# Performance work log

Measured on AMD Instinct MI355X. Metric: run time of the kernel, lower is better.

## Reference

```python
import jax, jax.numpy as jnp
import numpy as np

N = 30000      # nodes
E = 300000     # directed edges (self loops added in conv)
G = 128        # graphs in the batch
IN = 128       # input_dim
HID = 64       # hidden per head
HEADS = 4
NC = 10        # num_classes
EPS = 1e-5
SLOPE = 0.2    # GATv2 leaky_relu negative slope


def setup_inputs() -> dict:
    key = jax.random.key(0)
    ks = jax.random.split(key, 40)
    d = {}
    d['x'] = jax.random.normal(ks[0], (N, IN), jnp.float32)
    d['edge_index'] = jax.random.randint(ks[1], (2, E), 0, N, jnp.int32)
    d['batch'] = jnp.sort(jax.random.randint(ks[2], (N,), 0, G, jnp.int32))
    in_ch = [IN, HID * HEADS, HID * HEADS, HID * HEADS]
    for i in range(4):
        oc = HID * HEADS if i < 3 else HID  # last layer concat=False -> HID
        sc = 1.0 / np.sqrt(in_ch[i])
        d[f'Wl{i}'] = jax.random.normal(ks[3 + 6 * i], (in_ch[i], HID * HEADS), jnp.float32) * sc
        d[f'Wr{i}'] = jax.random.normal(ks[4 + 6 * i], (in_ch[i], HID * HEADS), jnp.float32) * sc
        d[f'att{i}'] = jax.random.normal(ks[5 + 6 * i], (HEADS, HID), jnp.float32) * 0.1
        d[f'b{i}'] = jnp.zeros((oc,), jnp.float32)
        d[f'bng{i}'] = jnp.ones((oc,), jnp.float32)
        d[f'bnb{i}'] = jnp.zeros((oc,), jnp.float32)
    d['fc1_w'] = jax.random.normal(ks[30], (HID, HID), jnp.float32) / np.sqrt(HID)
    d['fc1_b'] = jnp.zeros((HID,), jnp.float32)
    d['fc2_w'] = jax.random.normal(ks[31], (HID, NC), jnp.float32) / np.sqrt(HID)
    d['fc2_b'] = jnp.zeros((NC,), jnp.float32)
    return d


def _gatv2_conv(h, src, dst, Wl, Wr, att, b, concat):
    # GATv2Conv: x_l = lin_l(x) for sources, x_r = lin_r(x) for targets
    xl = (h @ Wl).reshape(N, HEADS, HID)
    xr = (h @ Wr).reshape(N, HEADS, HID)
    z = jax.nn.leaky_relu(xl[src] + xr[dst], SLOPE)       # [Et, H, C]
    e = jnp.einsum('ehc,hc->eh', z, att)                   # [Et, H]
    m = jax.ops.segment_max(e, dst, num_segments=N)        # per-dst max
    p = jnp.exp(e - m[dst])
    s = jax.ops.segment_sum(p, dst, num_segments=N)
    alpha = p / s[dst]                                     # segment softmax
    msg = alpha[..., None] * xl[src]                       # [Et, H, C]
    out = jax.ops.segment_sum(msg, dst, num_segments=N)    # [N, H, C]
    out = out.reshape(N, HEADS * HID) if concat else out.mean(axis=1)
    return out + b


def _bn_train(h, g, b):
    mu = h.mean(axis=0)
    var = h.var(axis=0)  # biased, as torch BN uses for normalization
    return g * (h - mu) * jax.lax.rsqrt(var + EPS) + b


def _forward(x, edge_index, batch,
             Wl0, Wr0, att0, b0, bng0, bnb0,
             Wl1, Wr1, att1, b1, bng1, bnb1,
             Wl2, Wr2, att2, b2, bng2, bnb2,
             Wl3, Wr3, att3, b3, bng3, bnb3,
             fc1_w, fc1_b, fc2_w, fc2_b):
    loops = jnp.arange(N, dtype=edge_index.dtype)
    src = jnp.concatenate([edge_index[0], loops])  # add_self_loops=True
    dst = jnp.concatenate([edge_index[1], loops])
    layers = [(Wl0, Wr0, att0, b0, bng0, bnb0, True),
              (Wl1, Wr1, att1, b1, bng1, bnb1, True),
              (Wl2, Wr2, att2, b2, bng2, bnb2, True),
              (Wl3, Wr3, att3, b3, bng3, bnb3, False)]
    h = x
    for Wl, Wr, att, b, g, bb, concat in layers:
        h = jax.nn.elu(_bn_train(_gatv2_conv(h, src, dst, Wl, Wr, att, b, concat), g, bb))
    sums = jax.ops.segment_sum(h, batch, num_segments=G)
    cnt = jax.ops.segment_sum(jnp.ones((N,), h.dtype), batch, num_segments=G)
    pooled = sums / jnp.maximum(cnt, 1.0)[:, None]         # global_mean_pool
    o = jax.nn.relu(pooled @ fc1_w + fc1_b)
    return o @ fc2_w + fc2_b                               # dropout off (eval)


def reference(x, edge_index, batch,
              Wl0, Wr0, att0, b0, bng0, bnb0,
              Wl1, Wr1, att1, b1, bng1, bnb1,
              Wl2, Wr2, att2, b2, bng2, bnb2,
              Wl3, Wr3, att3, b3, bng3, bnb3,
              fc1_w, fc1_b, fc2_w, fc2_b):
    return _forward(x, edge_index, batch,
                    Wl0, Wr0, att0, b0, bng0, bnb0,
                    Wl1, Wr1, att1, b1, bng1, bnb1,
                    Wl2, Wr2, att2, b2, bng2, bnb2,
                    Wl3, Wr3, att3, b3, bng3, bnb3,
                    fc1_w, fc1_b, fc2_w, fc2_b)
```

## Files before the change

kernel.cpp:

```cpp
#include <hip/hip_runtime.h>
#include <hip/hip_bf16.h>
#include <math.h>

#define NN    30000
#define EE    300000
#define ETOT  330000
#define GG    128
#define IND   128
#define HIDD  64
#define NHEAD 4
#define CC    256
#define NCL   10
#define EPSBN 1e-5f
#define SLOPE 0.2f

typedef __attribute__((ext_vector_type(8))) __bf16 bf16x8;
typedef __attribute__((ext_vector_type(4))) float f32x4;

__device__ inline float b2f(unsigned u16) {
    union { unsigned i; float f; } c; c.i = u16 << 16; return c.f;
}
__device__ inline unsigned short f2b(float f) {
    __hip_bfloat16 b = __float2bfloat16(f);
    unsigned short u; __builtin_memcpy(&u, &b, 2); return u;
}
__device__ inline void unpack8(uint4 u, float* f) {
    f[0] = b2f(u.x & 0xffffu); f[1] = b2f(u.x >> 16);
    f[2] = b2f(u.y & 0xffffu); f[3] = b2f(u.y >> 16);
    f[4] = b2f(u.z & 0xffffu); f[5] = b2f(u.z >> 16);
    f[6] = b2f(u.w & 0xffffu); f[7] = b2f(u.w >> 16);
}

__global__ void k_deg(const int* __restrict__ ei, int* __restrict__ deg) {
    int e = blockIdx.x * blockDim.x + threadIdx.x;
    if (e >= ETOT) return;
    int d = (e < EE) ? ei[EE + e] : (e - EE);
    atomicAdd(&deg[d], 1);
}

__global__ void k_scan(const int* __restrict__ deg, int* __restrict__ rowptr,
                       int* __restrict__ cursor) {
    const int PER = 30;
    int t = threadIdx.x;
    int base = t * PER;
    int loc[PER];
    int s = 0;
    #pragma unroll
    for (int j = 0; j < PER; ++j) {
        int v = (base + j < NN) ? deg[base + j] : 0;
        loc[j] = s; s += v;
    }
    int lane = t & 63, wid = t >> 6;
    int v = s;
    #pragma unroll
    for (int d = 1; d < 64; d <<= 1) {
        int u = __shfl_up(v, d, 64);
        if (lane >= d) v += u;
    }
    __shared__ int wsum[16], woff[16];
    if (lane == 63) wsum[wid] = v;
    __syncthreads();
    if (t == 0) { int a = 0; for (int w2 = 0; w2 < 16; ++w2) { woff[w2] = a; a += wsum[w2]; } }
    __syncthreads();
    int excl = woff[wid] + (v - s);
    #pragma unroll
    for (int j = 0; j < PER; ++j) {
        int idx = base + j;
        if (idx <= NN) { int val = excl + loc[j]; rowptr[idx] = val; cursor[idx] = val; }
    }
}

__global__ void k_scatter(const int* __restrict__ ei, int* __restrict__ cursor,
                          int* __restrict__ csrc) {
    int e = blockIdx.x * blockDim.x + threadIdx.x;
    if (e >= ETOT) return;
    int s, d;
    if (e < EE) { s = ei[e]; d = ei[EE + e]; } else { s = e - EE; d = s; }
    int pos = atomicAdd(&cursor[d], 1);
    csrc[pos] = s;
}

struct WPtrs { const float* wl[4]; const float* wr[4]; };

__global__ void k_prep(WPtrs p, const float* __restrict__ x,
                       __hip_bfloat16* __restrict__ wt, __hip_bfloat16* __restrict__ hb) {
    int id = blockIdx.x * 256 + threadIdx.x;
    if (id < 65536) {
        int n = id >> 7, k = id & 127;
        float v = (n < 256) ? p.wl[0][(size_t)k * 256 + n] : p.wr[0][(size_t)k * 256 + n - 256];
        wt[id] = __float2bfloat16(v);
    } else if (id < 458752) {
        int id2 = id - 65536;
        int li = 1 + (id2 >> 17);
        int r = id2 & 131071;
        int n = r >> 8, k = r & 255;
        float v = (n < 256) ? p.wl[li][(size_t)k * 256 + n] : p.wr[li][(size_t)k * 256 + n - 256];
        wt[id] = __float2bfloat16(v);
    } else {
        int id2 = id - 458752;
        if (id2 < NN * IND) hb[id2] = __float2bfloat16(x[id2]);
    }
}

template<int K>
__global__ __launch_bounds__(256) void k_gemm_mfma(
        const __hip_bfloat16* __restrict__ A, const __hip_bfloat16* __restrict__ Wt,
        __hip_bfloat16* __restrict__ xlb, __hip_bfloat16* __restrict__ xrb) {
    __shared__ __bf16 As[128 * 40];
    __shared__ __bf16 Bs[128 * 40];
    const int t = threadIdx.x;
    const int row0 = blockIdx.x * 128;
    const int col0 = blockIdx.y * 128;
    const int wv = t >> 6, lane = t & 63;
    const int wm = (wv & 1) * 64, wn = (wv >> 1) * 64;
    const int lm = lane & 15, lq = lane >> 4;
    f32x4 acc[4][4] = {};
    for (int k0 = 0; k0 < K; k0 += 32) {
        #pragma unroll
        for (int i = 0; i < 2; ++i) {
            int c = i * 256 + t;
            int r = c >> 2, cc = (c & 3) * 8;
            uint4 v = make_uint4(0u, 0u, 0u, 0u);
            int gr = row0 + r;
            if (gr < NN) v = *(const uint4*)&A[(size_t)gr * K + k0 + cc];
            *(uint4*)&As[r * 40 + cc] = v;
            uint4 w = *(const uint4*)&Wt[(size_t)(col0 + r) * K + k0 + cc];
            *(uint4*)&Bs[r * 40 + cc] = w;
        }
        __syncthreads();
        bf16x8 af[4], bfr[4];
        #pragma unroll
        for (int i = 0; i < 4; ++i) {
            af[i]  = *(bf16x8*)&As[(wm + i * 16 + lm) * 40 + lq * 8];
            bfr[i] = *(bf16x8*)&Bs[(wn + i * 16 + lm) * 40 + lq * 8];
        }
        #pragma unroll
        for (int i = 0; i < 4; ++i)
            #pragma unroll
            for (int j = 0; j < 4; ++j)
                acc[i][j] = __builtin_amdgcn_mfma_f32_16x16x32_bf16(af[i], bfr[j], acc[i][j], 0, 0, 0);
        __syncthreads();
    }
    const int crow = (lane >> 4) * 4;
    const int ccol = lane & 15;
    #pragma unroll
    for (int j = 0; j < 4; ++j) {
        int gcol = col0 + wn + j * 16 + ccol;
        __hip_bfloat16* O = (gcol < 256) ? xlb : xrb;
        int oc = (gcol < 256) ? gcol : gcol - 256;
        #pragma unroll
        for (int i = 0; i < 4; ++i) {
            #pragma unroll
            for (int r = 0; r < 4; ++r) {
                int grow = row0 + wm + i * 16 + crow + r;
                if (grow < NN) O[(size_t)grow * CC + oc] = __float2bfloat16(acc[i][j][r]);
            }
        }
    }
}

template<bool CONCAT>
__global__ __launch_bounds__(256) void k_gat(const __hip_bfloat16* __restrict__ xlb,
        const __hip_bfloat16* __restrict__ xrb, const int* __restrict__ rowptr,
        const int* __restrict__ csrc, const float* __restrict__ att,
        __hip_bfloat16* __restrict__ outb, float* __restrict__ outf) {
    const int wv = threadIdx.x >> 6, lane = threadIdx.x & 63;
    const int n = blockIdx.x * 4 + wv;
    if (n >= NN) return;
    const int sub = lane >> 5, l5 = lane & 31;
    const float4* att4 = (const float4*)att;
    float4 a0 = att4[l5 * 2], a1 = att4[l5 * 2 + 1];
    float aw[8] = {a0.x, a0.y, a0.z, a0.w, a1.x, a1.y, a1.z, a1.w};
    const uint4* xl4 = (const uint4*)xlb;
    const uint4* xr4 = (const uint4*)xrb;
    float xrv[8]; unpack8(xr4[(size_t)n * 32 + l5], xrv);
    const int beg = rowptr[n], end = rowptr[n + 1];
    float m = -1e30f, ssum = 0.f;
    float acc[8] = {};
    for (int i0 = beg; i0 < end; i0 += 2) {
        int i = i0 + sub;
        bool valid = i < end;
        int s = csrc[valid ? i : (end - 1)];
        float xlv[8]; unpack8(xl4[(size_t)s * 32 + l5], xlv);
        float tv = 0.f;
        #pragma unroll
        for (int j = 0; j < 8; ++j) {
            float v = xlv[j] + xrv[j];
            v = fmaxf(v, SLOPE * v);
            tv += v * aw[j];
        }
        tv += __shfl_xor(tv, 1);
        tv += __shfl_xor(tv, 2);
        tv += __shfl_xor(tv, 4);
        if (!valid) tv = -1e38f;
        float mn = fmaxf(m, tv);
        float sc = __expf(m - mn);
        float p  = __expf(tv - mn);
        ssum = ssum * sc + p;
        #pragma unroll
        for (int j = 0; j < 8; ++j) acc[j] = acc[j] * sc + p * xlv[j];
        m = mn;
    }
    float om = __shfl_xor(m, 32);
    float mn = fmaxf(m, om);
    float sa = __expf(m - mn), sb = __expf(om - mn);
    float osum = __shfl_xor(ssum, 32);
    ssum = ssum * sa + osum * sb;
    #pragma unroll
    for (int j = 0; j < 8; ++j) {
        float oa = __shfl_xor(acc[j], 32);
        acc[j] = acc[j] * sa + oa * sb;
    }
    float inv = 1.f / ssum;
    if (CONCAT) {
        if (sub == 0) {
            unsigned short r[8];
            #pragma unroll
            for (int j = 0; j < 8; ++j) r[j] = f2b(acc[j] * inv);
            uint4 o;
            o.x = r[0] | ((unsigned)r[1] << 16); o.y = r[2] | ((unsigned)r[3] << 16);
            o.z = r[4] | ((unsigned)r[5] << 16); o.w = r[6] | ((unsigned)r[7] << 16);
            ((uint4*)outb)[(size_t)n * 32 + l5] = o;
        }
    } else {
        float v[8];
        #pragma unroll
        for (int j = 0; j < 8; ++j) {
            v[j] = acc[j] * inv;
            v[j] += __shfl_xor(v[j], 8);
            v[j] += __shfl_xor(v[j], 16);
            v[j] *= 0.25f;
        }
        if (lane < 8) {
            ((float4*)outf)[(size_t)n * 16 + lane * 2]     = make_float4(v[0], v[1], v[2], v[3]);
            ((float4*)outf)[(size_t)n * 16 + lane * 2 + 1] = make_float4(v[4], v[5], v[6], v[7]);
        }
    }
}

__global__ __launch_bounds__(256) void k_bnstats256b(const __hip_bfloat16* __restrict__ in,
                                                     float* __restrict__ stats) {
    __shared__ float sh[512];
    int r0 = blockIdx.x * 128;
    int rend = min(r0 + 128, NN);
    int t = threadIdx.x;
    int half = t >> 7, tc = t & 127;
    float s0 = 0.f, s1 = 0.f, q0 = 0.f, q1 = 0.f;
    const unsigned* u32 = (const unsigned*)in;
    for (int r = r0 + half; r < rend; r += 2) {
        unsigned w = u32[(size_t)r * 128 + tc];
        float a = b2f(w & 0xffffu), b = b2f(w >> 16);
        s0 += a; q0 += a * a; s1 += b; q1 += b * b;
    }
    if (half) {
        sh[tc * 4 + 0] = s0; sh[tc * 4 + 1] = s1;
        sh[tc * 4 + 2] = q0; sh[tc * 4 + 3] = q1;
    }
    __syncthreads();
    if (!half) {
        s0 += sh[tc * 4 + 0]; s1 += sh[tc * 4 + 1];
        q0 += sh[tc * 4 + 2]; q1 += sh[tc * 4 + 3];
        atomicAdd(&stats[2 * tc], s0);       atomicAdd(&stats[2 * tc + 1], s1);
        atomicAdd(&stats[256 + 2 * tc], q0); atomicAdd(&stats[256 + 2 * tc + 1], q1);
    }
}

__global__ __launch_bounds__(256) void k_bnelu256b(const __hip_bfloat16* __restrict__ in,
        const float* __restrict__ stats, const float* __restrict__ gamma,
        const float* __restrict__ beta, __hip_bfloat16* __restrict__ outb) {
    int id = blockIdx.x * 256 + threadIdx.x;
    if (id >= NN * 32) return;
    int c0 = (id & 31) * 8;
    uint4 u = ((const uint4*)in)[id];
    float f[8]; unpack8(u, f);
    unsigned short r[8];
    #pragma unroll
    for (int j = 0; j < 8; ++j) {
        int c = c0 + j;
        float mu  = stats[c] * (1.f / NN);
        float var = stats[256 + c] * (1.f / NN) - mu * mu;
        float w = gamma[c] * rsqrtf(var + EPSBN);
        float v = w * (f[j] - mu) + beta[c];
        v = (v > 0.f) ? v : (__expf(v) - 1.f);
        r[j] = f2b(v);
    }
    uint4 o;
    o.x = r[0] | ((unsigned)r[1] << 16); o.y = r[2] | ((unsigned)r[3] << 16);
    o.z = r[4] | ((unsigned)r[5] << 16); o.w = r[6] | ((unsigned)r[7] << 16);
    ((uint4*)outb)[id] = o;
}

__global__ void k_bnstats64(const float* __restrict__ h, float* __restrict__ stats) {
    int r0 = blockIdx.x * 128;
    int rend = min(r0 + 128, NN);
    int c = threadIdx.x & 63;
    int ro = threadIdx.x >> 6;
    float s = 0.f, q = 0.f;
    for (int r = r0 + ro; r < rend; r += 4) {
        float v = h[(size_t)r * 64 + c];
        s += v; q += v * v;
    }
    atomicAdd(&stats[c], s); atomicAdd(&stats[64 + c], q);
}

__global__ void k_bnelu64(const float* __restrict__ in, const float* __restrict__ stats,
        const float* __restrict__ gamma, const float* __restrict__ beta,
        float* __restrict__ outf) {
    int i = blockIdx.x * blockDim.x + threadIdx.x;
    if (i >= NN * 64) return;
    int c = i & 63;
    float mu  = stats[c] * (1.f / NN);
    float var = stats[64 + c] * (1.f / NN) - mu * mu;
    float w = gamma[c] * rsqrtf(var + EPSBN);
    float v = w * (in[i] - mu) + beta[c];
    outf[i] = (v > 0.f) ? v : (__expf(v) - 1.f);
}

__global__ void k_pool(const float* __restrict__ h, const int* __restrict__ batch,
                       float* __restrict__ pooled, float* __restrict__ cnt) {
    int wv = threadIdx.x >> 6, lane = threadIdx.x & 63;
    int w = blockIdx.x * 4 + wv;
    int n0 = w * 64;
    if (n0 >= NN) return;
    int n1 = min(n0 + 64, NN);
    float sum = 0.f;
    int cur = batch[n0], c = 0;
    for (int n = n0; n < n1; ++n) {
        int g = batch[n];
        if (g != cur) {
            atomicAdd(&pooled[cur * 64 + lane], sum);
            if (lane == 0) atomicAdd(&cnt[cur], (float)c);
            sum = 0.f; c = 0; cur = g;
        }
        sum += h[(size_t)n * 64 + lane];
        ++c;
    }
    atomicAdd(&pooled[cur * 64 + lane], sum);
    if (lane == 0) atomicAdd(&cnt[cur], (float)c);
}

__global__ void k_mlp(const float* __restrict__ pooled, const float* __restrict__ cnt,
        const float* __restrict__ w1, const float* __restrict__ b1,
        const float* __restrict__ w2, const float* __restrict__ b2,
        float* __restrict__ out) {
    __shared__ float p[64], o[64];
    int g = blockIdx.x, t = threadIdx.x;
    float c = fmaxf(cnt[g], 1.f);
    p[t] = pooled[g * 64 + t] / c;
    __syncthreads();
    float s = b1[t];
    for (int k = 0; k < 64; ++k) s += p[k] * w1[k * 64 + t];
    o[t] = fmaxf(s, 0.f);
    __syncthreads();
    if (t < NCL) {
        float s2 = b2[t];
        for (int k = 0; k < 64; ++k) s2 += o[k] * w2[k * NCL + t];
        out[g * NCL + t] = s2;
    }
}

extern "C" void kernel_launch(void* const* d_in, const int* in_sizes, int n_in,
                              void* d_out, int out_size, void* d_ws, size_t ws_size,
                              hipStream_t stream) {
    const float* x     = (const float*)d_in[0];
    const int*   ei    = (const int*)d_in[1];
    const int*   batch = (const int*)d_in[2];
    WPtrs wp;
    const float *attp[4], *bng[4], *bnb[4];
    for (int i = 0; i < 4; ++i) {
        wp.wl[i] = (const float*)d_in[3 + 6 * i];
        wp.wr[i] = (const float*)d_in[4 + 6 * i];
        attp[i]  = (const float*)d_in[5 + 6 * i];
        bng[i]   = (const float*)d_in[7 + 6 * i];
        bnb[i]   = (const float*)d_in[8 + 6 * i];
    }
    const float* fc1w = (const float*)d_in[27];
    const float* fc1b = (const float*)d_in[28];
    const float* fc2w = (const float*)d_in[29];
    const float* fc2b = (const float*)d_in[30];
    float* out = (float*)d_out;

    char* w = (char*)d_ws;
    __hip_bfloat16* xlb = (__hip_bfloat16*)w; w += (size_t)NN * CC * 2;
    __hip_bfloat16* xrb = (__hip_bfloat16*)w; w += (size_t)NN * CC * 2;
    __hip_bfloat16* bufB = (__hip_bfloat16*)w; w += (size_t)NN * CC * 2;
    __hip_bfloat16* hb   = (__hip_bfloat16*)w; w += (size_t)NN * CC * 2;
    __hip_bfloat16* wt   = (__hip_bfloat16*)w; w += (size_t)458752 * 2;
    float* bufF   = (float*)w; w += (size_t)NN * HIDD * 4;
    float* bufA   = (float*)w; w += (size_t)NN * HIDD * 4;
    int*   rowptr = (int*)w;   w += (size_t)(NN + 1) * 4;
    int*   cursor = (int*)w;   w += (size_t)(NN + 1) * 4;
    int*   csrc   = (int*)w;   w += (size_t)ETOT * 4;
    char* zbase = w;
    int*   deg       = (int*)w;   w += (size_t)NN * 4;
    float* stats_all = (float*)w; w += (size_t)4 * 512 * 4;
    float* pooled    = (float*)w; w += (size_t)GG * HIDD * 4;
    float* cnt       = (float*)w; w += (size_t)GG * 4;
    size_t zbytes = (size_t)(w - zbase);

    __hip_bfloat16* Wt[4];
    Wt[0] = wt;
    Wt[1] = wt + 65536;
    Wt[2] = wt + 65536 + 131072;
    Wt[3] = wt + 65536 + 262144;

    hipMemsetAsync(zbase, 0, zbytes, stream);
    k_deg<<<(ETOT + 255) / 256, 256, 0, stream>>>(ei, deg);
    k_scan<<<1, 1024, 0, stream>>>(deg, rowptr, cursor);
    k_scatter<<<(ETOT + 255) / 256, 256, 0, stream>>>(ei, cursor, csrc);
    k_prep<<<(458752 + NN * IND + 255) / 256, 256, 0, stream>>>(wp, x, wt, hb);

    for (int L = 0; L < 4; ++L) {
        float* stats = stats_all + 512 * L;
        dim3 gg((NN + 127) / 128, 4);
        if (L == 0) k_gemm_mfma<IND><<<gg, 256, 0, stream>>>(hb, Wt[0], xlb, xrb);
        else        k_gemm_mfma<CC><<<gg, 256, 0, stream>>>(hb, Wt[L], xlb, xrb);
        if (L < 3) {
            k_gat<true><<<NN / 4, 256, 0, stream>>>(xlb, xrb, rowptr, csrc, attp[L], bufB, nullptr);
            k_bnstats256b<<<(NN + 127) / 128, 256, 0, stream>>>(bufB, stats);
            k_bnelu256b<<<(NN * 32 + 255) / 256, 256, 0, stream>>>(bufB, stats, bng[L], bnb[L], hb);
        } else {
            k_gat<false><<<NN / 4, 256, 0, stream>>>(xlb, xrb, rowptr, csrc, attp[3], nullptr, bufF);
            k_bnstats64<<<(NN + 127) / 128, 256, 0, stream>>>(bufF, stats);
            k_bnelu64<<<(NN * 64 + 255) / 256, 256, 0, stream>>>(bufF, stats, bng[3], bnb[3], bufA);
        }
    }
    k_pool<<<((NN + 63) / 64 + 3) / 4, 256, 0, stream>>>(bufA, batch, pooled, cnt);
    k_mlp<<<GG, 64, 0, stream>>>(pooled, cnt, fc1w, fc1b, fc2w, fc2b, out);
}
```

Measured before the change: 622.0 us.

## Prefetch GEMM tiles, drop softmax max-tracking, fuse final BN-ELU into pooling

The GEMM now prefetches the next K-slice into registers while the current one computes. Its buffers are padded to a multiple of 128 rows so the row bounds checks can be dropped, and the xl/xr output pointer is chosen once per block. The GAT kernel stops tracking a running max for the online softmax and sums exp(e) directly, which removes the rescaling exps and multiplies. This risks overflow if attention logits are large. The final BN+ELU is folded into the pooling kernel, which removes one elementwise kernel launch and one intermediate buffer.

```diff
diff --git a/kernel.cpp b/kernel.cpp
--- a/kernel.cpp
+++ b/kernel.cpp
@@ -3,6 +3,7 @@
 #include <math.h>
 
 #define NN    30000
+#define MPAD  30080
 #define EE    300000
 #define ETOT  330000
 #define GG    128
@@ -114,20 +115,27 @@
     const int wv = t >> 6, lane = t & 63;
     const int wm = (wv & 1) * 64, wn = (wv >> 1) * 64;
     const int lm = lane & 15, lq = lane >> 4;
+    const int sr0 = t >> 2, scc = (t & 3) * 8;
+    const int sr1 = sr0 + 64;
+    uint4 va0, va1, vb0, vb1;
+    va0 = *(const uint4*)&A [(size_t)(row0 + sr0) * K + scc];
+    va1 = *(const uint4*)&A [(size_t)(row0 + sr1) * K + scc];
+    vb0 = *(const uint4*)&Wt[(size_t)(col0 + sr0) * K + scc];
+    vb1 = *(const uint4*)&Wt[(size_t)(col0 + sr1) * K + scc];
     f32x4 acc[4][4] = {};
     for (int k0 = 0; k0 < K; k0 += 32) {
-        #pragma unroll
-        for (int i = 0; i < 2; ++i) {
-            int c = i * 256 + t;
-            int r = c >> 2, cc = (c & 3) * 8;
-            uint4 v = make_uint4(0u, 0u, 0u, 0u);
-            int gr = row0 + r;
-            if (gr < NN) v = *(const uint4*)&A[(size_t)gr * K + k0 + cc];
-            *(uint4*)&As[r * 40 + cc] = v;
-            uint4 w = *(const uint4*)&Wt[(size_t)(col0 + r) * K + k0 + cc];
-            *(uint4*)&Bs[r * 40 + cc] = w;
-        }
+        *(uint4*)&As[sr0 * 40 + scc] = va0;
+        *(uint4*)&As[sr1 * 40 + scc] = va1;
+        *(uint4*)&Bs[sr0 * 40 + scc] = vb0;
+        *(uint4*)&Bs[sr1 * 40 + scc] = vb1;
         __syncthreads();
+        if (k0 + 32 < K) {
+            int kn = k0 + 32;
+            va0 = *(const uint4*)&A [(size_t)(row0 + sr0) * K + kn + scc];
+            va1 = *(const uint4*)&A [(size_t)(row0 + sr1) * K + kn + scc];
+            vb0 = *(const uint4*)&Wt[(size_t)(col0 + sr0) * K + kn + scc];
+            vb1 = *(const uint4*)&Wt[(size_t)(col0 + sr1) * K + kn + scc];
+        }
         bf16x8 af[4], bfr[4];
         #pragma unroll
         for (int i = 0; i < 4; ++i) {
@@ -141,20 +149,18 @@
                 acc[i][j] = __builtin_amdgcn_mfma_f32_16x16x32_bf16(af[i], bfr[j], acc[i][j], 0, 0, 0);
         __syncthreads();
     }
-    const int crow = (lane >> 4) * 4;
-    const int ccol = lane & 15;
+    const int crow = lq * 4;
+    __hip_bfloat16* O = (blockIdx.y < 2) ? xlb : xrb;
+    const int cbase = (blockIdx.y & 1) * 128 + wn;
     #pragma unroll
     for (int j = 0; j < 4; ++j) {
-        int gcol = col0 + wn + j * 16 + ccol;
-        __hip_bfloat16* O = (gcol < 256) ? xlb : xrb;
-        int oc = (gcol < 256) ? gcol : gcol - 256;
+        int oc = cbase + j * 16 + lm;
         #pragma unroll
         for (int i = 0; i < 4; ++i) {
+            int grow = row0 + wm + i * 16 + crow;
             #pragma unroll
-            for (int r = 0; r < 4; ++r) {
-                int grow = row0 + wm + i * 16 + crow + r;
-                if (grow < NN) O[(size_t)grow * CC + oc] = __float2bfloat16(acc[i][j][r]);
-            }
+            for (int r = 0; r < 4; ++r)
+                O[(size_t)(grow + r) * CC + oc] = __float2bfloat16(acc[i][j][r]);
         }
     }
 }
@@ -175,42 +181,31 @@
     const uint4* xr4 = (const uint4*)xrb;
     float xrv[8]; unpack8(xr4[(size_t)n * 32 + l5], xrv);
     const int beg = rowptr[n], end = rowptr[n + 1];
-    float m = -1e30f, ssum = 0.f;
+    float ssum = 0.f;
     float acc[8] = {};
     for (int i0 = beg; i0 < end; i0 += 2) {
         int i = i0 + sub;
         bool valid = i < end;
-        int s = csrc[valid ? i : (end - 1)];
+        int s = csrc[valid ? i : end - 1];
         float xlv[8]; unpack8(xl4[(size_t)s * 32 + l5], xlv);
         float tv = 0.f;
         #pragma unroll
         for (int j = 0; j < 8; ++j) {
             float v = xlv[j] + xrv[j];
             v = fmaxf(v, SLOPE * v);
-            tv += v * aw[j];
+            tv = fmaf(v, aw[j], tv);
         }
         tv += __shfl_xor(tv, 1);
         tv += __shfl_xor(tv, 2);
         tv += __shfl_xor(tv, 4);
-        if (!valid) tv = -1e38f;
-        float mn = fmaxf(m, tv);
-        float sc = __expf(m - mn);
-        float p  = __expf(tv - mn);
-        ssum = ssum * sc + p;
-        #pragma unroll
-        for (int j = 0; j < 8; ++j) acc[j] = acc[j] * sc + p * xlv[j];
-        m = mn;
-    }
-    float om = __shfl_xor(m, 32);
-    float mn = fmaxf(m, om);
-    float sa = __expf(m - mn), sb = __expf(om - mn);
-    float osum = __shfl_xor(ssum, 32);
-    ssum = ssum * sa + osum * sb;
-    #pragma unroll
-    for (int j = 0; j < 8; ++j) {
-        float oa = __shfl_xor(acc[j], 32);
-        acc[j] = acc[j] * sa + oa * sb;
-    }
+        float p = valid ? __expf(tv) : 0.f;
+        ssum += p;
+        #pragma unroll
+        for (int j = 0; j < 8; ++j) acc[j] = fmaf(p, xlv[j], acc[j]);
+    }
+    ssum += __shfl_xor(ssum, 32);
+    #pragma unroll
+    for (int j = 0; j < 8; ++j) acc[j] += __shfl_xor(acc[j], 32);
     float inv = 1.f / ssum;
     if (CONCAT) {
         if (sub == 0) {
@@ -303,26 +298,19 @@
     atomicAdd(&stats[c], s); atomicAdd(&stats[64 + c], q);
 }
 
-__global__ void k_bnelu64(const float* __restrict__ in, const float* __restrict__ stats,
-        const float* __restrict__ gamma, const float* __restrict__ beta,
-        float* __restrict__ outf) {
-    int i = blockIdx.x * blockDim.x + threadIdx.x;
-    if (i >= NN * 64) return;
-    int c = i & 63;
-    float mu  = stats[c] * (1.f / NN);
-    float var = stats[64 + c] * (1.f / NN) - mu * mu;
-    float w = gamma[c] * rsqrtf(var + EPSBN);
-    float v = w * (in[i] - mu) + beta[c];
-    outf[i] = (v > 0.f) ? v : (__expf(v) - 1.f);
-}
-
 __global__ void k_pool(const float* __restrict__ h, const int* __restrict__ batch,
+                       const float* __restrict__ stats, const float* __restrict__ gamma,
+                       const float* __restrict__ beta,
                        float* __restrict__ pooled, float* __restrict__ cnt) {
     int wv = threadIdx.x >> 6, lane = threadIdx.x & 63;
     int w = blockIdx.x * 4 + wv;
     int n0 = w * 64;
     if (n0 >= NN) return;
     int n1 = min(n0 + 64, NN);
+    float mu  = stats[lane] * (1.f / NN);
+    float var = stats[64 + lane] * (1.f / NN) - mu * mu;
+    float sc = gamma[lane] * rsqrtf(var + EPSBN);
+    float sh = beta[lane] - mu * sc;
     float sum = 0.f;
     int cur = batch[n0], c = 0;
     for (int n = n0; n < n1; ++n) {
@@ -332,7 +320,9 @@
             if (lane == 0) atomicAdd(&cnt[cur], (float)c);
             sum = 0.f; c = 0; cur = g;
         }
-        sum += h[(size_t)n * 64 + lane];
+        float v = fmaf(h[(size_t)n * 64 + lane], sc, sh);
+        v = (v > 0.f) ? v : (__expf(v) - 1.f);
+        sum += v;
         ++c;
     }
     atomicAdd(&pooled[cur * 64 + lane], sum);
@@ -381,13 +371,12 @@
     float* out = (float*)d_out;
 
     char* w = (char*)d_ws;
-    __hip_bfloat16* xlb = (__hip_bfloat16*)w; w += (size_t)NN * CC * 2;
-    __hip_bfloat16* xrb = (__hip_bfloat16*)w; w += (size_t)NN * CC * 2;
-    __hip_bfloat16* bufB = (__hip_bfloat16*)w; w += (size_t)NN * CC * 2;
-    __hip_bfloat16* hb   = (__hip_bfloat16*)w; w += (size_t)NN * CC * 2;
+    __hip_bfloat16* xlb  = (__hip_bfloat16*)w; w += (size_t)MPAD * CC * 2;
+    __hip_bfloat16* xrb  = (__hip_bfloat16*)w; w += (size_t)MPAD * CC * 2;
+    __hip_bfloat16* bufB = (__hip_bfloat16*)w; w += (size_t)MPAD * CC * 2;
+    __hip_bfloat16* hb   = (__hip_bfloat16*)w; w += (size_t)MPAD * CC * 2;
     __hip_bfloat16* wt   = (__hip_bfloat16*)w; w += (size_t)458752 * 2;
     float* bufF   = (float*)w; w += (size_t)NN * HIDD * 4;
-    float* bufA   = (float*)w; w += (size_t)NN * HIDD * 4;
     int*   rowptr = (int*)w;   w += (size_t)(NN + 1) * 4;
     int*   cursor = (int*)w;   w += (size_t)(NN + 1) * 4;
     int*   csrc   = (int*)w;   w += (size_t)ETOT * 4;
@@ -412,7 +401,7 @@
 
     for (int L = 0; L < 4; ++L) {
         float* stats = stats_all + 512 * L;
-        dim3 gg((NN + 127) / 128, 4);
+        dim3 gg(MPAD / 128, 4);
         if (L == 0) k_gemm_mfma<IND><<<gg, 256, 0, stream>>>(hb, Wt[0], xlb, xrb);
         else        k_gemm_mfma<CC><<<gg, 256, 0, stream>>>(hb, Wt[L], xlb, xrb);
         if (L < 3) {
@@ -422,9 +411,9 @@
         } else {
             k_gat<false><<<NN / 4, 256, 0, stream>>>(xlb, xrb, rowptr, csrc, attp[3], nullptr, bufF);
             k_bnstats64<<<(NN + 127) / 128, 256, 0, stream>>>(bufF, stats);
-            k_bnelu64<<<(NN * 64 + 255) / 256, 256, 0, stream>>>(bufF, stats, bng[3], bnb[3], bufA);
-        }
-    }
-    k_pool<<<((NN + 63) / 64 + 3) / 4, 256, 0, stream>>>(bufA, batch, pooled, cnt);
+        }
+    }
+    k_pool<<<((NN + 63) / 64 + 3) / 4, 256, 0, stream>>>(bufF, batch, stats_all + 512 * 3,
+                                                         bng[3], bnb[3], pooled, cnt);
     k_mlp<<<GG, 64, 0, stream>>>(pooled, cnt, fc1w, fc1b, fc2w, fc2b, out);
 }
```

After: 599.0 us. -3.7%, faster.
